# Optimization experiments

Hardware: AMD Instinct MI355X
Metric: run time of the kernel (lower is better)

Reference implementation:

```python
import jax, jax.numpy as jnp
import numpy as np

NUM_POSITIONS = 4096
EMBED_DIM = 512
BSZ, SEQ_LEN = 16, 4096


def setup_inputs() -> dict:
    key = jax.random.key(0)
    k1, k2 = jax.random.split(key)
    input_tensor = jax.random.normal(k1, (BSZ, SEQ_LEN, EMBED_DIM), dtype=jnp.float32)
    pv = jax.random.normal(k2, (NUM_POSITIONS, EMBED_DIM), dtype=jnp.float32)
    # L2-normalize each position vector (as in _init_position_vectors)
    pv = pv / jnp.linalg.norm(pv, axis=1, keepdims=True)
    return {"input_tensor": input_tensor, "position_vectors": pv}


def reference(input_tensor, position_vectors):
    # input_tensor: [B, S, D]; position_vectors: [P, D] with S <= P.
    seq_len, d = input_tensor.shape[1], input_tensor.shape[-1]
    pos = position_vectors[:seq_len]  # [S, D]
    # Batched circular convolution over the last axis via rFFT.
    x_fft = jnp.fft.rfft(input_tensor, axis=-1)          # [B, S, D//2+1] complex
    p_fft = jnp.fft.rfft(pos, axis=-1)[None, :, :]       # [1, S, D//2+1]
    out = jnp.fft.irfft(x_fft * p_fft, n=d, axis=-1)     # [B, S, D]
    return out.astype(input_tensor.dtype)
```

## Files before the change

### kernel.cpp

```cpp
#include <hip/hip_runtime.h>
#include <math.h>

#ifndef M_PI
#define M_PI 3.14159265358979323846
#endif

#define BSZ 16
#define SEQ 4096
#define DIM 512

#define REG_SZ 656

__device__ __forceinline__ float2 cadd(float2 a, float2 b){ return make_float2(a.x+b.x, a.y+b.y); }
__device__ __forceinline__ float2 csub(float2 a, float2 b){ return make_float2(a.x-b.x, a.y-b.y); }
__device__ __forceinline__ float2 cmul(float2 a, float2 b){
  return make_float2(fmaf(a.x, b.x, -(a.y*b.y)), fmaf(a.x, b.y, a.y*b.x));
}
__device__ __forceinline__ float2 cmulc(float2 a, float2 b){
  return make_float2(fmaf(a.x, b.x, a.y*b.y), fmaf(a.y, b.x, -(a.x*b.y)));
}
__device__ __forceinline__ float2 mul_mi(float2 a){ return make_float2(a.y, -a.x); }

__device__ __forceinline__ void dft8(const float2* in, float2* out){
  float2 t0 = cadd(in[0], in[4]), t1 = csub(in[0], in[4]);
  float2 t2 = cadd(in[2], in[6]), t3 = csub(in[2], in[6]);
  float2 E0 = cadd(t0, t2), E2 = csub(t0, t2);
  float2 m3 = mul_mi(t3);
  float2 E1 = cadd(t1, m3), E3 = csub(t1, m3);
  float2 s0 = cadd(in[1], in[5]), s1 = csub(in[1], in[5]);
  float2 s2 = cadd(in[3], in[7]), s3 = csub(in[3], in[7]);
  float2 O0 = cadd(s0, s2), O2 = csub(s0, s2);
  float2 n3 = mul_mi(s3);
  float2 O1 = cadd(s1, n3), O3 = csub(s1, n3);
  const float C = 0.70710678118654752440f;
  float2 w1o = make_float2(C*(O1.x + O1.y), C*(O1.y - O1.x));
  float2 w2o = mul_mi(O2);
  float2 w3o = make_float2(C*(O3.y - O3.x), -(C*(O3.x + O3.y)));
  out[0] = cadd(E0, O0); out[4] = csub(E0, O0);
  out[1] = cadd(E1, w1o); out[5] = csub(E1, w1o);
  out[2] = cadd(E2, w2o); out[6] = csub(E2, w2o);
  out[3] = cadd(E3, w3o); out[7] = csub(E3, w3o);
}

__device__ __forceinline__ void idft8(const float2* in, float2* out){
  float2 t[8];
  dft8(in, t);
  out[0]=t[0]; out[1]=t[7]; out[2]=t[6]; out[3]=t[5];
  out[4]=t[4]; out[5]=t[3]; out[6]=t[2]; out[7]=t[1];
}

__device__ __forceinline__ void fft512_fwd(float2* v, float2* lds, int lane,
                                           const float2* wA, const float2* wB){
  const int a = lane >> 3, b = lane & 7;
  float2 t[8];
  dft8(v, t);
  #pragma unroll
  for (int r = 1; r < 8; ++r) t[r] = cmul(t[r], wA[r]);
  __syncthreads();
  #pragma unroll
  for (int r = 0; r < 8; ++r) lds[72*r + lane] = t[r];
  __syncthreads();
  #pragma unroll
  for (int j2 = 0; j2 < 8; ++j2) v[j2] = lds[72*a + b + 8*j2];
  dft8(v, t);
  #pragma unroll
  for (int r2 = 1; r2 < 8; ++r2) t[r2] = cmul(t[r2], wB[r2]);
  __syncthreads();
  #pragma unroll
  for (int r2 = 0; r2 < 8; ++r2) lds[a + 82*r2 + 10*b] = t[r2];
  __syncthreads();
  #pragma unroll
  for (int i2 = 0; i2 < 8; ++i2) v[i2] = lds[a + 82*b + 10*i2];
  dft8(v, t);
  #pragma unroll
  for (int m = 0; m < 8; ++m) v[m] = t[m];
}

__device__ __forceinline__ void fft512_inv(float2* v, float2* lds, int lane,
                                           const float2* wA, const float2* wB){
  const int a = lane >> 3, b = lane & 7;
  float2 t[8];
  idft8(v, t);
  __syncthreads();
  #pragma unroll
  for (int i2 = 0; i2 < 8; ++i2) lds[a + 82*b + 10*i2] = t[i2];
  __syncthreads();
  #pragma unroll
  for (int r2 = 0; r2 < 8; ++r2) v[r2] = lds[a + 82*r2 + 10*b];
  #pragma unroll
  for (int r2 = 1; r2 < 8; ++r2) v[r2] = cmulc(v[r2], wB[r2]);
  idft8(v, t);
  __syncthreads();
  #pragma unroll
  for (int j2 = 0; j2 < 8; ++j2) lds[72*a + b + 8*j2] = t[j2];
  __syncthreads();
  #pragma unroll
  for (int r = 0; r < 8; ++r) v[r] = lds[72*r + lane];
  #pragma unroll
  for (int r = 1; r < 8; ++r) v[r] = cmulc(v[r], wA[r]);
  idft8(v, t);
  #pragma unroll
  for (int j = 0; j < 8; ++j) v[j] = t[j];
}

__global__ void __launch_bounds__(256)
circconv_kernel(const float* __restrict__ x, const float* __restrict__ p,
                float* __restrict__ out){
  __shared__ float2 lds_all[4 * REG_SZ];
  const int lane = threadIdx.x & 63;
  const int wid  = threadIdx.x >> 6;
  float2* lds = lds_all + wid * REG_SZ;

  const int g    = blockIdx.x * 4 + wid;
  const int s    = g >> 1;
  const int half = g & 1;
  const int b    = lane & 7;

  float2 wA[8], wB[8];
  wA[0] = make_float2(1.f, 0.f); wB[0] = make_float2(1.f, 0.f);
  #pragma unroll
  for (int r = 1; r < 8; ++r){
    float sv, cv;
    sincosf(-2.0f*(float)M_PI*(float)(lane*r)*(1.0f/512.0f), &sv, &cv);
    wA[r] = make_float2(cv, sv);
    sincosf(-2.0f*(float)M_PI*(float)(b*r)*(1.0f/64.0f), &sv, &cv);
    wB[r] = make_float2(cv, sv);
  }

  float2 pf[8];
  {
    const float* prow = p + (size_t)s * DIM;
    #pragma unroll
    for (int j = 0; j < 8; ++j) pf[j] = make_float2(prow[lane + 64*j], 0.f);
    fft512_fwd(pf, lds, lane, wA, wB);
    #pragma unroll
    for (int m = 0; m < 8; ++m){ pf[m].x *= (1.0f/512.0f); pf[m].y *= (1.0f/512.0f); }
  }

  const int b_lo = half * 8;
  for (int bb = b_lo; bb < b_lo + 8; bb += 2){
    const size_t base0 = ((size_t)bb       * SEQ + s) * DIM;
    const size_t base1 = ((size_t)(bb + 1) * SEQ + s) * DIM;
    float2 v[8];
    #pragma unroll
    for (int j = 0; j < 8; ++j)
      v[j] = make_float2(x[base0 + lane + 64*j], x[base1 + lane + 64*j]);
    fft512_fwd(v, lds, lane, wA, wB);
    #pragma unroll
    for (int m = 0; m < 8; ++m) v[m] = cmul(v[m], pf[m]);
    fft512_inv(v, lds, lane, wA, wB);
    #pragma unroll
    for (int j = 0; j < 8; ++j){
      out[base0 + lane + 64*j] = v[j].x;
      out[base1 + lane + 64*j] = v[j].y;
    }
  }
}

extern "C" void kernel_launch(void* const* d_in, const int* in_sizes, int n_in,
                              void* d_out, int out_size, void* d_ws, size_t ws_size,
                              hipStream_t stream) {
  (void)in_sizes; (void)n_in; (void)d_ws; (void)ws_size; (void)out_size;
  const float* x  = (const float*)d_in[0];
  const float* p  = (const float*)d_in[1];
  float* o        = (float*)d_out;
  circconv_kernel<<<SEQ*2/4, 256, 0, stream>>>(x, p, o);
}
```

Before: 243.0 us.

## Use single-wave blocks processing two FFT pairs at once with early loads

Each block is now one 64-lane wave instead of four waves sharing a block, so __syncthreads only synchronizes a single wave. The FFT stages are interleaved across two independent complex pairs (four batch rows) to raise instruction-level parallelism. The first x loads are issued before the position FFT so their latency is hidden. This costs more registers per thread and doubles the LDS per wave, which can reduce occupancy.

```diff
diff --git a/kernel.cpp b/kernel.cpp
--- a/kernel.cpp
+++ b/kernel.cpp
@@ -49,6 +49,7 @@
   out[4]=t[4]; out[5]=t[3]; out[6]=t[2]; out[7]=t[1];
 }
 
+
 __device__ __forceinline__ void fft512_fwd(float2* v, float2* lds, int lane,
                                            const float2* wA, const float2* wB){
   const int a = lane >> 3, b = lane & 7;
@@ -76,42 +77,81 @@
   for (int m = 0; m < 8; ++m) v[m] = t[m];
 }
 
-__device__ __forceinline__ void fft512_inv(float2* v, float2* lds, int lane,
-                                           const float2* wA, const float2* wB){
+__device__ __forceinline__ void fft512_fwd2(float2* va, float2* vb,
+                                            float2* ldsA, float2* ldsB, int lane,
+                                            const float2* wA, const float2* wB){
   const int a = lane >> 3, b = lane & 7;
-  float2 t[8];
-  idft8(v, t);
-  __syncthreads();
-  #pragma unroll
-  for (int i2 = 0; i2 < 8; ++i2) lds[a + 82*b + 10*i2] = t[i2];
-  __syncthreads();
-  #pragma unroll
-  for (int r2 = 0; r2 < 8; ++r2) v[r2] = lds[a + 82*r2 + 10*b];
-  #pragma unroll
-  for (int r2 = 1; r2 < 8; ++r2) v[r2] = cmulc(v[r2], wB[r2]);
-  idft8(v, t);
-  __syncthreads();
-  #pragma unroll
-  for (int j2 = 0; j2 < 8; ++j2) lds[72*a + b + 8*j2] = t[j2];
-  __syncthreads();
-  #pragma unroll
-  for (int r = 0; r < 8; ++r) v[r] = lds[72*r + lane];
-  #pragma unroll
-  for (int r = 1; r < 8; ++r) v[r] = cmulc(v[r], wA[r]);
-  idft8(v, t);
-  #pragma unroll
-  for (int j = 0; j < 8; ++j) v[j] = t[j];
-}
-
-__global__ void __launch_bounds__(256)
+  float2 ta[8], tb[8];
+  dft8(va, ta);
+  #pragma unroll
+  for (int r = 1; r < 8; ++r) ta[r] = cmul(ta[r], wA[r]);
+  dft8(vb, tb);
+  #pragma unroll
+  for (int r = 1; r < 8; ++r) tb[r] = cmul(tb[r], wA[r]);
+  __syncthreads();
+  #pragma unroll
+  for (int r = 0; r < 8; ++r){ ldsA[72*r + lane] = ta[r]; ldsB[72*r + lane] = tb[r]; }
+  __syncthreads();
+  #pragma unroll
+  for (int j2 = 0; j2 < 8; ++j2){ va[j2] = ldsA[72*a + b + 8*j2]; vb[j2] = ldsB[72*a + b + 8*j2]; }
+  dft8(va, ta);
+  #pragma unroll
+  for (int r2 = 1; r2 < 8; ++r2) ta[r2] = cmul(ta[r2], wB[r2]);
+  dft8(vb, tb);
+  #pragma unroll
+  for (int r2 = 1; r2 < 8; ++r2) tb[r2] = cmul(tb[r2], wB[r2]);
+  __syncthreads();
+  #pragma unroll
+  for (int r2 = 0; r2 < 8; ++r2){ ldsA[a + 82*r2 + 10*b] = ta[r2]; ldsB[a + 82*r2 + 10*b] = tb[r2]; }
+  __syncthreads();
+  #pragma unroll
+  for (int i2 = 0; i2 < 8; ++i2){ va[i2] = ldsA[a + 82*b + 10*i2]; vb[i2] = ldsB[a + 82*b + 10*i2]; }
+  dft8(va, ta); dft8(vb, tb);
+  #pragma unroll
+  for (int m = 0; m < 8; ++m){ va[m] = ta[m]; vb[m] = tb[m]; }
+}
+
+__device__ __forceinline__ void fft512_inv2(float2* va, float2* vb,
+                                            float2* ldsA, float2* ldsB, int lane,
+                                            const float2* wA, const float2* wB){
+  const int a = lane >> 3, b = lane & 7;
+  float2 ta[8], tb[8];
+  idft8(va, ta); idft8(vb, tb);
+  __syncthreads();
+  #pragma unroll
+  for (int i2 = 0; i2 < 8; ++i2){ ldsA[a + 82*b + 10*i2] = ta[i2]; ldsB[a + 82*b + 10*i2] = tb[i2]; }
+  __syncthreads();
+  #pragma unroll
+  for (int r2 = 0; r2 < 8; ++r2){ va[r2] = ldsA[a + 82*r2 + 10*b]; vb[r2] = ldsB[a + 82*r2 + 10*b]; }
+  #pragma unroll
+  for (int r2 = 1; r2 < 8; ++r2) va[r2] = cmulc(va[r2], wB[r2]);
+  idft8(va, ta);
+  #pragma unroll
+  for (int r2 = 1; r2 < 8; ++r2) vb[r2] = cmulc(vb[r2], wB[r2]);
+  idft8(vb, tb);
+  __syncthreads();
+  #pragma unroll
+  for (int j2 = 0; j2 < 8; ++j2){ ldsA[72*a + b + 8*j2] = ta[j2]; ldsB[72*a + b + 8*j2] = tb[j2]; }
+  __syncthreads();
+  #pragma unroll
+  for (int r = 0; r < 8; ++r){ va[r] = ldsA[72*r + lane]; vb[r] = ldsB[72*r + lane]; }
+  #pragma unroll
+  for (int r = 1; r < 8; ++r) va[r] = cmulc(va[r], wA[r]);
+  idft8(va, ta);
+  #pragma unroll
+  for (int r = 1; r < 8; ++r) vb[r] = cmulc(vb[r], wA[r]);
+  idft8(vb, tb);
+  #pragma unroll
+  for (int j = 0; j < 8; ++j){ va[j] = ta[j]; vb[j] = tb[j]; }
+}
+
+__global__ void __launch_bounds__(64, 4)
 circconv_kernel(const float* __restrict__ x, const float* __restrict__ p,
                 float* __restrict__ out){
-  __shared__ float2 lds_all[4 * REG_SZ];
-  const int lane = threadIdx.x & 63;
-  const int wid  = threadIdx.x >> 6;
-  float2* lds = lds_all + wid * REG_SZ;
-
-  const int g    = blockIdx.x * 4 + wid;
+  __shared__ float2 ldsA[REG_SZ];
+  __shared__ float2 ldsB[REG_SZ];
+  const int lane = threadIdx.x;
+  const int g    = blockIdx.x;
   const int s    = g >> 1;
   const int half = g & 1;
   const int b    = lane & 7;
@@ -127,32 +167,55 @@
     wB[r] = make_float2(cv, sv);
   }
 
+  const int b_lo = half * 8;
+  const size_t sbase = (size_t)s * DIM + lane;
+  float2 va[8], vb[8];
+  {
+    const size_t r0 = ((size_t)(b_lo+0) * SEQ) * DIM + sbase;
+    const size_t r1 = ((size_t)(b_lo+1) * SEQ) * DIM + sbase;
+    const size_t r2 = ((size_t)(b_lo+2) * SEQ) * DIM + sbase;
+    const size_t r3 = ((size_t)(b_lo+3) * SEQ) * DIM + sbase;
+    #pragma unroll
+    for (int j = 0; j < 8; ++j){
+      va[j] = make_float2(x[r0 + 64*j], x[r1 + 64*j]);
+      vb[j] = make_float2(x[r2 + 64*j], x[r3 + 64*j]);
+    }
+  }
+
   float2 pf[8];
   {
     const float* prow = p + (size_t)s * DIM;
     #pragma unroll
     for (int j = 0; j < 8; ++j) pf[j] = make_float2(prow[lane + 64*j], 0.f);
-    fft512_fwd(pf, lds, lane, wA, wB);
+    fft512_fwd(pf, ldsA, lane, wA, wB);
     #pragma unroll
     for (int m = 0; m < 8; ++m){ pf[m].x *= (1.0f/512.0f); pf[m].y *= (1.0f/512.0f); }
   }
 
-  const int b_lo = half * 8;
-  for (int bb = b_lo; bb < b_lo + 8; bb += 2){
-    const size_t base0 = ((size_t)bb       * SEQ + s) * DIM;
-    const size_t base1 = ((size_t)(bb + 1) * SEQ + s) * DIM;
-    float2 v[8];
-    #pragma unroll
-    for (int j = 0; j < 8; ++j)
-      v[j] = make_float2(x[base0 + lane + 64*j], x[base1 + lane + 64*j]);
-    fft512_fwd(v, lds, lane, wA, wB);
-    #pragma unroll
-    for (int m = 0; m < 8; ++m) v[m] = cmul(v[m], pf[m]);
-    fft512_inv(v, lds, lane, wA, wB);
+  #pragma unroll
+  for (int q = 0; q < 2; ++q){
+    const int bb = b_lo + 4*q;
+    const size_t r0 = ((size_t)(bb+0) * SEQ) * DIM + sbase;
+    const size_t r1 = ((size_t)(bb+1) * SEQ) * DIM + sbase;
+    const size_t r2 = ((size_t)(bb+2) * SEQ) * DIM + sbase;
+    const size_t r3 = ((size_t)(bb+3) * SEQ) * DIM + sbase;
+    if (q > 0){
+      #pragma unroll
+      for (int j = 0; j < 8; ++j){
+        va[j] = make_float2(x[r0 + 64*j], x[r1 + 64*j]);
+        vb[j] = make_float2(x[r2 + 64*j], x[r3 + 64*j]);
+      }
+    }
+    fft512_fwd2(va, vb, ldsA, ldsB, lane, wA, wB);
+    #pragma unroll
+    for (int m = 0; m < 8; ++m){ va[m] = cmul(va[m], pf[m]); vb[m] = cmul(vb[m], pf[m]); }
+    fft512_inv2(va, vb, ldsA, ldsB, lane, wA, wB);
     #pragma unroll
     for (int j = 0; j < 8; ++j){
-      out[base0 + lane + 64*j] = v[j].x;
-      out[base1 + lane + 64*j] = v[j].y;
+      out[r0 + 64*j] = va[j].x;
+      out[r1 + 64*j] = va[j].y;
+      out[r2 + 64*j] = vb[j].x;
+      out[r3 + 64*j] = vb[j].y;
     }
   }
 }
@@ -164,5 +227,5 @@
   const float* x  = (const float*)d_in[0];
   const float* p  = (const float*)d_in[1];
   float* o        = (float*)d_out;
-  circconv_kernel<<<SEQ*2/4, 256, 0, stream>>>(x, p, o);
-}
+  circconv_kernel<<<SEQ*2, 64, 0, stream>>>(x, p, o);
+}
```

Result: slower. 302.6 us (+24.5%).
